# Optimization experiments

Measured on AMD Instinct MI355X. Metric: run time of the kernel, lower is better.

## Reference

```python
import jax, jax.numpy as jnp
import numpy as np

B, T, C, K = 4, 8192, 2048, 4


def setup_inputs() -> dict:
    key = jax.random.key(0)
    kx, kw, kb = jax.random.split(key, 3)
    x = jax.random.normal(kx, (B, T, C), dtype=jnp.float32)
    # depthwise kernel, HIO layout: [K, 1, C]; matches torch Conv1d weight [C,1,K] transposed
    bound = 1.0 / np.sqrt(K)  # torch Conv1d default init: U(-1/sqrt(fan_in)), fan_in = K for depthwise
    weight = jax.random.uniform(kw, (K, 1, C), dtype=jnp.float32, minval=-bound, maxval=bound)
    bias = jax.random.uniform(kb, (C,), dtype=jnp.float32, minval=-bound, maxval=bound)
    return {"x": x, "weight": weight, "bias": bias}


def reference(x, weight, bias):
    # Causal depthwise conv1d in NHC layout: left-pad K-1, no transposes needed.
    # out[b, t, c] = bias[c] + sum_k weight[k, 0, c] * x[b, t - (K-1) + k, c]
    out = jax.lax.conv_general_dilated(
        x, weight,
        window_strides=(1,),
        padding=[(weight.shape[0] - 1, 0)],
        dimension_numbers=("NHC", "HIO", "NHC"),
        feature_group_count=x.shape[-1],
    )
    return out + bias
```

## Files before the change

### kernel.cpp

```cpp
#include <hip/hip_runtime.h>


constexpr int B = 4;
constexpr int T = 8192;
constexpr int C = 2048;
constexpr int C4 = C / 4;
constexpr int TCHUNK = 8;
constexpr int NCHUNK = T / TCHUNK;
constexpr int NLOAD = TCHUNK + 3;

__global__ __launch_bounds__(256) void causal_conv1d_kernel(
    const float4* __restrict__ x,
    const float*  __restrict__ w,
    const float*  __restrict__ bias,
    float4* __restrict__ out)
{
    const int idx  = blockIdx.x * blockDim.x + threadIdx.x;
    const int c4   = idx & (C4 - 1);
    const int rest = idx >> 9;
    const int tc   = rest & (NCHUNK - 1);
    const int b    = rest >> 10;
    const int t0   = tc * TCHUNK;

    const float4* xb = x   + (size_t)b * T * C4;
    float4*       ob = out + (size_t)b * T * C4;

    const float4 zero = make_float4(0.f, 0.f, 0.f, 0.f);
    float4 xv[NLOAD];

    if (t0 != 0) {
#pragma unroll
        for (int i = 0; i < NLOAD; ++i)
            xv[i] = xb[(size_t)(t0 - 3 + i) * C4 + c4];
    } else {
        xv[0] = zero; xv[1] = zero; xv[2] = zero;
#pragma unroll
        for (int i = 3; i < NLOAD; ++i)
            xv[i] = xb[(size_t)(t0 - 3 + i) * C4 + c4];
    }

    const float4* w4 = (const float4*)w;
    const float4 w0 = w4[0 * C4 + c4];
    const float4 w1 = w4[1 * C4 + c4];
    const float4 w2 = w4[2 * C4 + c4];
    const float4 w3 = w4[3 * C4 + c4];
    const float4 bs = ((const float4*)bias)[c4];

#pragma unroll
    for (int j = 0; j < TCHUNK; ++j) {
        const float4 a0 = xv[j], a1 = xv[j + 1], a2 = xv[j + 2], a3 = xv[j + 3];
        float4 o;
        o.x = fmaf(w3.x, a3.x, fmaf(w2.x, a2.x, fmaf(w1.x, a1.x, fmaf(w0.x, a0.x, bs.x))));
        o.y = fmaf(w3.y, a3.y, fmaf(w2.y, a2.y, fmaf(w1.y, a1.y, fmaf(w0.y, a0.y, bs.y))));
        o.z = fmaf(w3.z, a3.z, fmaf(w2.z, a2.z, fmaf(w1.z, a1.z, fmaf(w0.z, a0.z, bs.z))));
        o.w = fmaf(w3.w, a3.w, fmaf(w2.w, a2.w, fmaf(w1.w, a1.w, fmaf(w0.w, a0.w, bs.w))));
        ob[(size_t)(t0 + j) * C4 + c4] = o;
    }
}

extern "C" void kernel_launch(void* const* d_in, const int* in_sizes, int n_in,
                              void* d_out, int out_size, void* d_ws, size_t ws_size,
                              hipStream_t stream) {
    const float4* x    = (const float4*)d_in[0];
    const float*  w    = (const float*)d_in[1];
    const float*  bias = (const float*)d_in[2];
    float4* out = (float4*)d_out;

    const int total_threads = B * NCHUNK * C4;
    const int block = 256;
    const int grid = total_threads / block;
    causal_conv1d_kernel<<<grid, block, 0, stream>>>(x, w, bias, out);
}
```

Before: 437.4 us.

## Process 64-step time strips per thread with sliding window and prefetch

Each thread now covers a 64-timestep strip instead of 8 steps. It keeps a sliding register window so the 3-element halo is reloaded once per strip rather than once per 8 steps, and it prefetches the next 8 inputs while computing the current chunk. This cuts redundant halo loads and the per-thread weight and bias loads. In exchange the grid is 8x smaller and register pressure is higher, which can lower occupancy and latency hiding on a memory-bound kernel.

```diff
diff --git a/kernel.cpp b/kernel.cpp
--- a/kernel.cpp
+++ b/kernel.cpp
@@ -6,8 +6,9 @@
 constexpr int C = 2048;
 constexpr int C4 = C / 4;
 constexpr int TCHUNK = 8;
-constexpr int NCHUNK = T / TCHUNK;
-constexpr int NLOAD = TCHUNK + 3;
+constexpr int LSTRIP = 64;
+constexpr int NSTEPS = LSTRIP / TCHUNK;
+constexpr int NSTRIP = T / LSTRIP;
 
 __global__ __launch_bounds__(256) void causal_conv1d_kernel(
     const float4* __restrict__ x,
@@ -18,26 +19,12 @@
     const int idx  = blockIdx.x * blockDim.x + threadIdx.x;
     const int c4   = idx & (C4 - 1);
     const int rest = idx >> 9;
-    const int tc   = rest & (NCHUNK - 1);
-    const int b    = rest >> 10;
-    const int t0   = tc * TCHUNK;
+    const int s    = rest & (NSTRIP - 1);
+    const int b    = rest >> 7;
+    const int t0   = s * LSTRIP;
 
     const float4* xb = x   + (size_t)b * T * C4;
     float4*       ob = out + (size_t)b * T * C4;
-
-    const float4 zero = make_float4(0.f, 0.f, 0.f, 0.f);
-    float4 xv[NLOAD];
-
-    if (t0 != 0) {
-#pragma unroll
-        for (int i = 0; i < NLOAD; ++i)
-            xv[i] = xb[(size_t)(t0 - 3 + i) * C4 + c4];
-    } else {
-        xv[0] = zero; xv[1] = zero; xv[2] = zero;
-#pragma unroll
-        for (int i = 3; i < NLOAD; ++i)
-            xv[i] = xb[(size_t)(t0 - 3 + i) * C4 + c4];
-    }
 
     const float4* w4 = (const float4*)w;
     const float4 w0 = w4[0 * C4 + c4];
@@ -46,15 +33,51 @@
     const float4 w3 = w4[3 * C4 + c4];
     const float4 bs = ((const float4*)bias)[c4];
 
+    const float4 zero = make_float4(0.f, 0.f, 0.f, 0.f);
+
+    float4 win[TCHUNK + 3];
+
+    if (t0 != 0) {
 #pragma unroll
-    for (int j = 0; j < TCHUNK; ++j) {
-        const float4 a0 = xv[j], a1 = xv[j + 1], a2 = xv[j + 2], a3 = xv[j + 3];
-        float4 o;
-        o.x = fmaf(w3.x, a3.x, fmaf(w2.x, a2.x, fmaf(w1.x, a1.x, fmaf(w0.x, a0.x, bs.x))));
-        o.y = fmaf(w3.y, a3.y, fmaf(w2.y, a2.y, fmaf(w1.y, a1.y, fmaf(w0.y, a0.y, bs.y))));
-        o.z = fmaf(w3.z, a3.z, fmaf(w2.z, a2.z, fmaf(w1.z, a1.z, fmaf(w0.z, a0.z, bs.z))));
-        o.w = fmaf(w3.w, a3.w, fmaf(w2.w, a2.w, fmaf(w1.w, a1.w, fmaf(w0.w, a0.w, bs.w))));
-        ob[(size_t)(t0 + j) * C4 + c4] = o;
+        for (int i = 0; i < TCHUNK + 3; ++i)
+            win[i] = xb[(size_t)(t0 - 3 + i) * C4 + c4];
+    } else {
+        win[0] = zero; win[1] = zero; win[2] = zero;
+#pragma unroll
+        for (int i = 0; i < TCHUNK; ++i)
+            win[3 + i] = xb[(size_t)i * C4 + c4];
+    }
+
+#pragma unroll
+    for (int step = 0; step < NSTEPS; ++step) {
+        const int tbase = t0 + step * TCHUNK;
+
+        float4 nxt[TCHUNK];
+        if (step < NSTEPS - 1) {
+#pragma unroll
+            for (int i = 0; i < TCHUNK; ++i)
+                nxt[i] = xb[(size_t)(tbase + TCHUNK + i) * C4 + c4];
+        }
+
+#pragma unroll
+        for (int j = 0; j < TCHUNK; ++j) {
+            const float4 a0 = win[j], a1 = win[j + 1], a2 = win[j + 2], a3 = win[j + 3];
+            float4 o;
+            o.x = fmaf(w3.x, a3.x, fmaf(w2.x, a2.x, fmaf(w1.x, a1.x, fmaf(w0.x, a0.x, bs.x))));
+            o.y = fmaf(w3.y, a3.y, fmaf(w2.y, a2.y, fmaf(w1.y, a1.y, fmaf(w0.y, a0.y, bs.y))));
+            o.z = fmaf(w3.z, a3.z, fmaf(w2.z, a2.z, fmaf(w1.z, a1.z, fmaf(w0.z, a0.z, bs.z))));
+            o.w = fmaf(w3.w, a3.w, fmaf(w2.w, a2.w, fmaf(w1.w, a1.w, fmaf(w0.w, a0.w, bs.w))));
+            ob[(size_t)(tbase + j) * C4 + c4] = o;
+        }
+
+        if (step < NSTEPS - 1) {
+            win[0] = win[TCHUNK];
+            win[1] = win[TCHUNK + 1];
+            win[2] = win[TCHUNK + 2];
+#pragma unroll
+            for (int i = 0; i < TCHUNK; ++i)
+                win[3 + i] = nxt[i];
+        }
     }
 }
 
@@ -66,7 +89,7 @@
     const float*  bias = (const float*)d_in[2];
     float4* out = (float4*)d_out;
 
-    const int total_threads = B * NCHUNK * C4;
+    const int total_threads = B * NSTRIP * C4;
     const int block = 256;
     const int grid = total_threads / block;
     causal_conv1d_kernel<<<grid, block, 0, stream>>>(x, w, bias, out);
```

Measured after the change: 436.4 us. Within noise of the previous version (-0.2%).
